# Kernel tuning notes

Measured on AMD Instinct MI355X. Metric: run time of the kernel, lower is better.

Reference implementation:

```python
import jax, jax.numpy as jnp
import numpy as np

DIM = 3
EPS = 1e-6

def _u(r):
    # radial basis: r^2 * log(r + eps)
    return r * r * jnp.log(r + EPS)

def _pairdist(a, b):
    # (N,T,d),(N,S,d) -> (N,T,S); small T so direct broadcast is fine
    return jnp.sqrt(jnp.sum((a[:, :, None, :] - b[:, None, :, :]) ** 2, -1) + EPS)

def _fit(ctrl, tgt, lmbda):
    # Solve [K + lmbda*I, P; P^T, 0] [w;a] = [tgt;0]
    N, T, _ = ctrl.shape
    dt = ctrl.dtype
    K = _u(_pairdist(ctrl, ctrl)) + jnp.eye(T, dtype=dt) * lmbda[:, None, None]
    P = jnp.concatenate([jnp.ones((N, T, 1), dt), ctrl], -1)  # (N,T,4)
    M = T + DIM + 1
    A = jnp.zeros((N, M, M), dt)
    A = A.at[:, :T, :T].set(K)
    A = A.at[:, :T, T:].set(P)
    A = A.at[:, T:, :T].set(jnp.swapaxes(P, 1, 2))
    v = jnp.zeros((N, M), dt).at[:, :T].set(tgt)
    return jnp.linalg.solve(A, v[..., None])[..., 0]  # (N, T+4)

def _uniform_grid(N, D, H, W, dt):
    # homogeneous coord first; coord1 varies over W, coord2 over H, coord3 over D
    c1 = jnp.broadcast_to(jnp.linspace(-1, 1, W, dtype=dt)[None, None, :], (D, H, W))
    c2 = jnp.broadcast_to(jnp.linspace(-1, 1, H, dtype=dt)[None, :, None], (D, H, W))
    c3 = jnp.broadcast_to(jnp.linspace(-1, 1, D, dtype=dt)[:, None, None], (D, H, W))
    g = jnp.stack([jnp.ones((D, H, W), dt), c1, c2, c3], -1)  # (D,H,W,4)
    return jnp.broadcast_to(g[None], (N, D, H, W, DIM + 1))

def setup_inputs() -> dict:
    key = jax.random.key(0)
    k1, k2, k3 = jax.random.split(key, 3)
    N, T = 2, 128
    points_m = jax.random.uniform(k1, (N, T, DIM), dtype=jnp.float32)
    points_f = jax.random.uniform(k2, (N, T, DIM), dtype=jnp.float32)
    lmbda = jax.random.uniform(k3, (N,), dtype=jnp.float32)
    return {"points_m": points_m, "points_f": points_f, "lmbda": lmbda,
            "D": 64, "H": 64, "W": 64}

def reference(points_m, points_f, lmbda, D, H, W):
    N, T, _ = points_f.shape
    # theta: fit per output coordinate; ctrl = points_f, targets = points_m
    theta = jnp.stack([_fit(points_f, points_m[..., k], lmbda) for k in range(DIM)], -1)  # (N,T+4,3)
    grid = _uniform_grid(N, D, H, W, points_f.dtype)
    g = grid.reshape(N, -1, DIM + 1)          # (N,P,4), P = D*H*W
    gc = g[..., 1:]                            # (N,P,3)
    # squared distances via expansion (avoids (N,P,T,3) blow-up)
    r2 = (jnp.sum(gc * gc, -1)[..., None]
          + jnp.sum(points_f * points_f, -1)[:, None, :]
          - 2.0 * jnp.einsum('npd,ntd->npt', gc, points_f))
    r = jnp.sqrt(jnp.maximum(r2, 0.0) + EPS)
    U = _u(r)                                  # (N,P,T)
    w, a = theta[:, :T, :], theta[:, T:, :]
    z = jnp.einsum('npt,ntd->npd', U, w) + jnp.einsum('npk,nkd->npd', g, a)
    return z.reshape(N, D, H, W, DIM)
```

## Files before the change

### kernel.cpp

```cpp
#include <hip/hip_runtime.h>

#define TPTS 128
#define MM   132
#define ST   136
#define NC4  34
#define NT   512
#define NPAN 17
#define TEPS 1e-6f
#define HLN2 0.34657359027997264f

__device__ __forceinline__ float rdlanef(float v, int l) {
    return __int_as_float(__builtin_amdgcn_readlane(__float_as_int(v), l));
}

__global__ __launch_bounds__(NT) void tps_fit(
    const float* __restrict__ pm,
    const float* __restrict__ pf,
    const float* __restrict__ lmb,
    float* __restrict__ theta)
{
    extern __shared__ float smem[];
    float*  Mf   = smem;
    float4* M4   = reinterpret_cast<float4*>(smem);
    float*  invd = smem + MM*ST;
    float*  sc   = invd + 132;
    float*  sg   = sc + TPTS*3;
    float*  dsc  = sg + TPTS*3;
    float4* dsc4 = reinterpret_cast<float4*>(dsc);

    const int n    = blockIdx.x;
    const int tid  = threadIdx.x;
    const int wid  = tid >> 6;
    const int lane = tid & 63;

    for (int i = tid; i < TPTS*3; i += NT) {
        sc[i] = pf[n*TPTS*3 + i];
        sg[i] = pm[n*TPTS*3 + i];
    }
    __syncthreads();
    const float lam = lmb[n];

    for (int q = tid; q < MM*NC4; q += NT) {
        const int row = q / NC4;
        const int cg  = q - row*NC4;
        float vv[4];
        #pragma unroll
        for (int e = 0; e < 4; ++e) {
            const int col = cg*4 + e;
            float v = 0.0f;
            if (col < TPTS) {
                if (row < TPTS) {
                    const float dx = sc[row*3+0] - sc[col*3+0];
                    const float dy = sc[row*3+1] - sc[col*3+1];
                    const float dz = sc[row*3+2] - sc[col*3+2];
                    const float r2 = fmaf(dx,dx, fmaf(dy,dy, fmaf(dz,dz, TEPS)));
                    v = 0.5f * r2 * __logf(r2);
                    if (row == col) v += lam;
                } else {
                    const int ci = row - TPTS;
                    v = (ci == 0) ? 1.0f : sc[col*3 + ci - 1];
                }
            } else if (col < MM) {
                if (row < TPTS) {
                    const int ci = col - TPTS;
                    v = (ci == 0) ? 1.0f : sc[row*3 + ci - 1];
                }
            } else if (col < MM + 3) {
                if (row < TPTS) v = sg[row*3 + (col - MM)];
            }
            vv[e] = v;
        }
        M4[q] = make_float4(vv[0], vv[1], vv[2], vv[3]);
    }
    __syncthreads();

    for (int p = 0; p < NPAN; ++p) {
        const int j0    = p*8;
        const int kb    = (MM - j0 >= 8) ? 8 : (MM - j0);
        const int cb    = j0 >> 2;
        const int RB    = (MM > j0 + 8) ? (MM - (j0 + 8)) : 0;
        const int ncols = 136 - (j0 + 8);

        const bool needD = (tid < RB) || (tid >= 128 && tid < 128 + ncols)
                                      || (tid >= 384 && tid < 392);
        if (needD) {
            float d[8][8]; float rd[8];
            #pragma unroll
            for (int m = 0; m < 8; ++m) {
                if (m < kb) {
                    float4 a = M4[(j0+m)*NC4+cb], b = M4[(j0+m)*NC4+cb+1];
                    d[m][0]=a.x; d[m][1]=a.y; d[m][2]=a.z; d[m][3]=a.w;
                    d[m][4]=b.x; d[m][5]=b.y; d[m][6]=b.z; d[m][7]=b.w;
                } else {
                    #pragma unroll
                    for (int c = 0; c < 8; ++c) d[m][c] = 0.0f;
                }
            }
            #pragma unroll
            for (int k = 0; k < 8; ++k) {
                if (k < kb) {
                    rd[k] = __builtin_amdgcn_rcpf(d[k][k]);
                    #pragma unroll
                    for (int i = 0; i < 8; ++i) {
                        if (i > k && i < kb) {
                            const float l = d[i][k] * rd[k];
                            d[i][k] = l;
                            #pragma unroll
                            for (int c = 0; c < 8; ++c) { if (c > k) d[i][c] = fmaf(-l, d[k][c], d[i][c]); }
                        }
                    }
                } else {
                    rd[k] = 1.0f;
                }
            }
            if (tid < RB) {
                const int row = j0 + 8 + tid;
                float4 a = M4[row*NC4+cb], b = M4[row*NC4+cb+1];
                float av[8] = {a.x,a.y,a.z,a.w,b.x,b.y,b.z,b.w};
                float l[8];
                #pragma unroll
                for (int c = 0; c < 8; ++c) {
                    float v = av[c];
                    #pragma unroll
                    for (int k = 0; k < 8; ++k) { if (k < c) v = fmaf(-l[k], d[k][c], v); }
                    l[c] = v * rd[c];
                }
                M4[row*NC4+cb]   = make_float4(l[0],l[1],l[2],l[3]);
                M4[row*NC4+cb+1] = make_float4(l[4],l[5],l[6],l[7]);
            } else if (tid >= 128 && tid < 128 + ncols) {
                const int col = j0 + 8 + (tid - 128);
                float s[8];
                #pragma unroll
                for (int m = 0; m < 8; ++m) s[m] = Mf[(j0+m)*ST + col];
                #pragma unroll
                for (int m = 1; m < 8; ++m) {
                    #pragma unroll
                    for (int k = 0; k < 8; ++k) { if (k < m) s[m] = fmaf(-d[m][k], s[k], s[m]); }
                }
                #pragma unroll
                for (int m = 0; m < 8; ++m) Mf[(j0+m)*ST + col] = s[m];
            } else {
                const int m = tid - 384;
                float rowv[8];
                #pragma unroll
                for (int mm = 0; mm < 8; ++mm) {
                    #pragma unroll
                    for (int c = 0; c < 8; ++c) { if (mm == m) rowv[c] = d[mm][c]; }
                }
                float rdm = 1.0f;
                #pragma unroll
                for (int mm = 0; mm < 8; ++mm) { if (mm == m) rdm = rd[mm]; }
                dsc4[m*2+0] = make_float4(rowv[0],rowv[1],rowv[2],rowv[3]);
                dsc4[m*2+1] = make_float4(rowv[4],rowv[5],rowv[6],rowv[7]);
                dsc[64+m]   = rdm;
            }
        }
        __syncthreads();

        if (tid >= 256 && tid < 264) {
            const int m = tid - 256;
            if (m < kb) {
                M4[(j0+m)*NC4+cb]   = dsc4[m*2+0];
                M4[(j0+m)*NC4+cb+1] = dsc4[m*2+1];
                invd[j0+m] = dsc[64+m];
            }
        }
        if (RB > 0) {
            const int cg0 = (j0 + 8) >> 2;
            const int ncg = NC4 - cg0;
            const int tpc = NT / ncg;
            const int tcg = tid % ncg, trow = tid / ncg;
            if (trow < tpc) {
                const int cg = cg0 + tcg;
                float4 u[8];
                #pragma unroll
                for (int m = 0; m < 8; ++m) u[m] = M4[(j0+m)*NC4 + cg];
                int i = j0 + 8 + trow;
                for (; i + tpc < MM; i += 2*tpc) {
                    const int ib = i + tpc;
                    const float4 la0 = M4[i *NC4+cb], lb0 = M4[i *NC4+cb+1];
                    const float4 la1 = M4[ib*NC4+cb], lb1 = M4[ib*NC4+cb+1];
                    float4 a0 = M4[i*NC4+cg], a1 = M4[ib*NC4+cg];
                    const float c0[8] = {la0.x,la0.y,la0.z,la0.w,lb0.x,lb0.y,lb0.z,lb0.w};
                    const float c1[8] = {la1.x,la1.y,la1.z,la1.w,lb1.x,lb1.y,lb1.z,lb1.w};
                    #pragma unroll
                    for (int m = 0; m < 8; ++m) {
                        a0.x = fmaf(-c0[m], u[m].x, a0.x); a0.y = fmaf(-c0[m], u[m].y, a0.y);
                        a0.z = fmaf(-c0[m], u[m].z, a0.z); a0.w = fmaf(-c0[m], u[m].w, a0.w);
                        a1.x = fmaf(-c1[m], u[m].x, a1.x); a1.y = fmaf(-c1[m], u[m].y, a1.y);
                        a1.z = fmaf(-c1[m], u[m].z, a1.z); a1.w = fmaf(-c1[m], u[m].w, a1.w);
                    }
                    M4[i *NC4+cg] = a0;
                    M4[ib*NC4+cg] = a1;
                }
                if (i < MM) {
                    const float4 la = M4[i*NC4+cb], lb = M4[i*NC4+cb+1];
                    float4 a0 = M4[i*NC4+cg];
                    const float c0[8] = {la.x,la.y,la.z,la.w,lb.x,lb.y,lb.z,lb.w};
                    #pragma unroll
                    for (int m = 0; m < 8; ++m) {
                        a0.x = fmaf(-c0[m], u[m].x, a0.x); a0.y = fmaf(-c0[m], u[m].y, a0.y);
                        a0.z = fmaf(-c0[m], u[m].z, a0.z); a0.w = fmaf(-c0[m], u[m].w, a0.w);
                    }
                    M4[i*NC4+cg] = a0;
                }
            }
        }
        __syncthreads();
    }

    if (wid == 0) {
        const int o0 = lane, o1 = lane + 64, o2 = lane + 128;
        float b0x,b0y,b0z, b1x,b1y,b1z, b2x=0,b2y=0,b2z=0;
        { float4 f = M4[o0*NC4 + 33]; b0x=f.x; b0y=f.y; b0z=f.z; }
        { float4 f = M4[o1*NC4 + 33]; b1x=f.x; b1y=f.y; b1z=f.z; }
        if (o2 < MM) { float4 f = M4[o2*NC4 + 33]; b2x=f.x; b2y=f.y; b2z=f.z; }
        float uc0 = Mf[o0*ST + (MM-1)];
        float uc1 = Mf[o1*ST + (MM-1)];
        float uc2 = (o2 < MM) ? Mf[o2*ST + (MM-1)] : 0.0f;
        float dvc = invd[MM-1];
        for (int j = MM - 1; j >= 0; --j) {
            float un0 = 0.f, un1 = 0.f, un2 = 0.f, dvn = 0.f;
            if (j > 0) {
                un0 = Mf[o0*ST + j-1];
                un1 = Mf[o1*ST + j-1];
                un2 = (o2 < MM) ? Mf[o2*ST + j-1] : 0.0f;
                dvn = invd[j-1];
            }
            const int jr = j >> 6, jl = j & 63;
            float s0, s1, s2;
            if (jr == 0)      { s0 = b0x; s1 = b0y; s2 = b0z; }
            else if (jr == 1) { s0 = b1x; s1 = b1y; s2 = b1z; }
            else              { s0 = b2x; s1 = b2y; s2 = b2z; }
            const float x0 = rdlanef(s0, jl) * dvc;
            const float x1 = rdlanef(s1, jl) * dvc;
            const float x2 = rdlanef(s2, jl) * dvc;
            if (o0 < j) { b0x = fmaf(-uc0,x0,b0x); b0y = fmaf(-uc0,x1,b0y); b0z = fmaf(-uc0,x2,b0z); }
            if (o1 < j) { b1x = fmaf(-uc1,x0,b1x); b1y = fmaf(-uc1,x1,b1y); b1z = fmaf(-uc1,x2,b1z); }
            if (o2 < j && o2 < MM) { b2x = fmaf(-uc2,x0,b2x); b2y = fmaf(-uc2,x1,b2y); b2z = fmaf(-uc2,x2,b2z); }
            if (lane == jl) {
                const float scale = (j < TPTS) ? HLN2 : 1.0f;
                theta[n*MM*3 + j*3 + 0] = x0 * scale;
                theta[n*MM*3 + j*3 + 1] = x1 * scale;
                theta[n*MM*3 + j*3 + 2] = x2 * scale;
            }
            uc0 = un0; uc1 = un1; uc2 = un2; dvc = dvn;
        }
    }
}

__global__ __launch_bounds__(256) void tps_eval(
    const float* __restrict__ pf,
    const float* __restrict__ theta,
    float* __restrict__ out)
{
    const int b   = blockIdx.x;
    const int n   = b >> 10;
    const int rem = ((b & 1023) << 8) | threadIdx.x;
    const int d = rem >> 12;
    const int h = (rem >> 6) & 63;
    const int w = rem & 63;
    const float stepv = 2.0f / 63.0f;
    const float gx = fmaf((float)w, stepv, -1.0f);
    const float gy = fmaf((float)h, stepv, -1.0f);
    const float gz = fmaf((float)d, stepv, -1.0f);

    const float* __restrict__ c  = pf    + n * TPTS * 3;
    const float* __restrict__ th = theta + n * MM * 3;

    float a0 = 0.f, a1 = 0.f, a2 = 0.f;
    #pragma unroll 8
    for (int t = 0; t < TPTS; ++t) {
        const float dx = gx - c[t*3+0];
        const float dy = gy - c[t*3+1];
        const float dz = gz - c[t*3+2];
        const float r2 = fmaf(dx,dx, fmaf(dy,dy, fmaf(dz,dz, TEPS)));
        const float lg = __log2f(r2);
        const float u  = r2 * lg;
        a0 = fmaf(u, th[t*3+0], a0);
        a1 = fmaf(u, th[t*3+1], a1);
        a2 = fmaf(u, th[t*3+2], a2);
    }
    const float* aa = th + TPTS*3;
    a0 = fmaf(gz, aa[9],  fmaf(gy, aa[6], fmaf(gx, aa[3], a0 + aa[0])));
    a1 = fmaf(gz, aa[10], fmaf(gy, aa[7], fmaf(gx, aa[4], a1 + aa[1])));
    a2 = fmaf(gz, aa[11], fmaf(gy, aa[8], fmaf(gx, aa[5], a2 + aa[2])));

    const long pid = (long)b * 256 + threadIdx.x;
    out[pid*3+0] = a0;
    out[pid*3+1] = a1;
    out[pid*3+2] = a2;
}

extern "C" void kernel_launch(void* const* d_in, const int* in_sizes, int n_in,
                              void* d_out, int out_size, void* d_ws, size_t ws_size,
                              hipStream_t stream) {
    (void)n_in; (void)out_size; (void)ws_size;
    const float* pm = (const float*)d_in[0];
    const float* pf = (const float*)d_in[1];
    const float* lm = (const float*)d_in[2];
    float* outp  = (float*)d_out;
    float* theta = (float*)d_ws;

    const int N = in_sizes[2];
    const size_t lds = (size_t)(MM*ST + 132 + TPTS*3*2 + 72) * sizeof(float);

    (void)hipFuncSetAttribute(reinterpret_cast<const void*>(tps_fit),
                              hipFuncAttributeMaxDynamicSharedMemorySize, (int)lds);

    tps_fit<<<N, NT, lds, stream>>>(pm, pf, lm, theta);
    tps_eval<<<N * 1024, 256, 0, stream>>>(pf, theta, outp);
}
```

Before: 99.64 us.

## Parallelize back-substitution across three waves using row-dot DPP reductions

The triangular back-substitution in the fit kernel used to run on a single wavefront in column-oriented form, broadcasting each solved value with readlane and updating all remaining right-hand sides. It now splits the three output coordinates across three waves. Each wave computes a row-oriented dot product of the solved values with the current row, reduces it with DPP row shifts and readlanes, and solves one unknown per step. This divides the serial work per wave by three and reads rows contiguously, but every step now carries a reduction latency chain and the loop is still serial over 132 steps.

```diff
diff --git a/kernel.cpp b/kernel.cpp
--- a/kernel.cpp
+++ b/kernel.cpp
@@ -9,8 +9,16 @@
 #define TEPS 1e-6f
 #define HLN2 0.34657359027997264f
 
-__device__ __forceinline__ float rdlanef(float v, int l) {
-    return __int_as_float(__builtin_amdgcn_readlane(__float_as_int(v), l));
+__device__ __forceinline__ float wred_sum64(float v) {
+    v += __int_as_float(__builtin_amdgcn_update_dpp(0, __float_as_int(v), 0x111, 0xF, 0xF, true));
+    v += __int_as_float(__builtin_amdgcn_update_dpp(0, __float_as_int(v), 0x112, 0xF, 0xF, true));
+    v += __int_as_float(__builtin_amdgcn_update_dpp(0, __float_as_int(v), 0x114, 0xF, 0xF, true));
+    v += __int_as_float(__builtin_amdgcn_update_dpp(0, __float_as_int(v), 0x118, 0xF, 0xF, true));
+    const float r0 = __int_as_float(__builtin_amdgcn_readlane(__float_as_int(v), 15));
+    const float r1 = __int_as_float(__builtin_amdgcn_readlane(__float_as_int(v), 31));
+    const float r2 = __int_as_float(__builtin_amdgcn_readlane(__float_as_int(v), 47));
+    const float r3 = __int_as_float(__builtin_amdgcn_readlane(__float_as_int(v), 63));
+    return (r0 + r1) + (r2 + r3);
 }
 
 __global__ __launch_bounds__(NT) void tps_fit(
@@ -209,42 +217,37 @@
         __syncthreads();
     }
 
-    if (wid == 0) {
-        const int o0 = lane, o1 = lane + 64, o2 = lane + 128;
-        float b0x,b0y,b0z, b1x,b1y,b1z, b2x=0,b2y=0,b2z=0;
-        { float4 f = M4[o0*NC4 + 33]; b0x=f.x; b0y=f.y; b0z=f.z; }
-        { float4 f = M4[o1*NC4 + 33]; b1x=f.x; b1y=f.y; b1z=f.z; }
-        if (o2 < MM) { float4 f = M4[o2*NC4 + 33]; b2x=f.x; b2y=f.y; b2z=f.z; }
-        float uc0 = Mf[o0*ST + (MM-1)];
-        float uc1 = Mf[o1*ST + (MM-1)];
-        float uc2 = (o2 < MM) ? Mf[o2*ST + (MM-1)] : 0.0f;
-        float dvc = invd[MM-1];
+    if (wid < 3) {
+        const int q = wid;
+        const int l = lane;
+        float x0 = 0.f, x1 = 0.f, x2 = 0.f;
+        float u0 = Mf[131*ST + l];
+        float u1 = Mf[131*ST + 64 + l];
+        float u2 = (l < 4) ? Mf[131*ST + 128 + l] : 0.0f;
+        float bc = Mf[131*ST + 132 + q];
+        float dc = invd[131];
         for (int j = MM - 1; j >= 0; --j) {
-            float un0 = 0.f, un1 = 0.f, un2 = 0.f, dvn = 0.f;
+            float n0 = 0.f, n1 = 0.f, n2 = 0.f, nb = 0.f, nd = 0.f;
             if (j > 0) {
-                un0 = Mf[o0*ST + j-1];
-                un1 = Mf[o1*ST + j-1];
-                un2 = (o2 < MM) ? Mf[o2*ST + j-1] : 0.0f;
-                dvn = invd[j-1];
-            }
-            const int jr = j >> 6, jl = j & 63;
-            float s0, s1, s2;
-            if (jr == 0)      { s0 = b0x; s1 = b0y; s2 = b0z; }
-            else if (jr == 1) { s0 = b1x; s1 = b1y; s2 = b1z; }
-            else              { s0 = b2x; s1 = b2y; s2 = b2z; }
-            const float x0 = rdlanef(s0, jl) * dvc;
-            const float x1 = rdlanef(s1, jl) * dvc;
-            const float x2 = rdlanef(s2, jl) * dvc;
-            if (o0 < j) { b0x = fmaf(-uc0,x0,b0x); b0y = fmaf(-uc0,x1,b0y); b0z = fmaf(-uc0,x2,b0z); }
-            if (o1 < j) { b1x = fmaf(-uc1,x0,b1x); b1y = fmaf(-uc1,x1,b1y); b1z = fmaf(-uc1,x2,b1z); }
-            if (o2 < j && o2 < MM) { b2x = fmaf(-uc2,x0,b2x); b2y = fmaf(-uc2,x1,b2y); b2z = fmaf(-uc2,x2,b2z); }
-            if (lane == jl) {
+                n0 = Mf[(j-1)*ST + l];
+                n1 = Mf[(j-1)*ST + 64 + l];
+                n2 = (l < 4) ? Mf[(j-1)*ST + 128 + l] : 0.0f;
+                nb = Mf[(j-1)*ST + 132 + q];
+                nd = invd[j-1];
+            }
+            float t = (l > j) ? u0 * x0 : 0.0f;
+            t = fmaf((64 + l > j) ? u1 : 0.0f, x1, t);
+            t = fmaf((l < 4 && 128 + l > j) ? u2 : 0.0f, x2, t);
+            const float dot = wred_sum64(t);
+            const float xj  = (bc - dot) * dc;
+            if (j >= 128)     { if (l == j - 128) x2 = xj; }
+            else if (j >= 64) { if (l == j - 64)  x1 = xj; }
+            else              { if (l == j)       x0 = xj; }
+            if (l == 0) {
                 const float scale = (j < TPTS) ? HLN2 : 1.0f;
-                theta[n*MM*3 + j*3 + 0] = x0 * scale;
-                theta[n*MM*3 + j*3 + 1] = x1 * scale;
-                theta[n*MM*3 + j*3 + 2] = x2 * scale;
-            }
-            uc0 = un0; uc1 = un1; uc2 = un2; dvc = dvn;
+                theta[n*MM*3 + j*3 + q] = xj * scale;
+            }
+            u0 = n0; u1 = n1; u2 = n2; bc = nb; dc = nd;
         }
     }
 }
```

Result: slower. 105.5 us (+5.8%).
